# Kernel tuning notes

Measured on AMD Instinct MI355X. Metric: run time of the kernel, lower is better.

The kernel has to match this reference:

```python
import jax, jax.numpy as jnp
import numpy as np

N_QUBITS = 10
N_QLAYERS = 2
EMBED = 1024
B, S = 16, 1024
DIM = 2 ** N_QUBITS


def _apply_rx(state, theta, w, n):
    # state: [N, 2^n] complex; RX(theta) on wire w (wire 0 = most significant bit)
    nb = state.shape[0]
    left, right = 2 ** w, 2 ** (n - 1 - w)
    psi = state.reshape(nb, left, 2, right)
    t = jnp.asarray(theta, jnp.float32) * 0.5
    c, s = jnp.cos(t), jnp.sin(t)
    if c.ndim == 1:  # per-sample angles
        c, s = c[:, None, None], s[:, None, None]
    a0, a1 = psi[:, :, 0, :], psi[:, :, 1, :]
    n0 = c * a0 - 1j * s * a1
    n1 = -1j * s * a0 + c * a1
    return jnp.stack([n0, n1], axis=2).reshape(nb, -1)


def _apply_cnot(state, c, t, n):
    # CNOT with control wire c, target wire t
    psi = state.reshape((-1,) + (2,) * n)
    ctrl_ax, tgt_ax = c + 1, t + 1
    psi0, psi1 = jnp.split(psi, 2, axis=ctrl_ax)
    psi1 = jnp.flip(psi1, axis=tgt_ax)
    return jnp.concatenate([psi0, psi1], axis=ctrl_ax).reshape(state.shape)


def setup_inputs() -> dict:
    key = jax.random.key(0)
    ks = jax.random.split(key, 6)
    s1 = 1.0 / np.sqrt(EMBED)
    s2 = 1.0 / np.sqrt(N_QUBITS)
    return {
        "x": jax.random.normal(ks[0], (B, S, EMBED), jnp.float32),
        "W1": jax.random.uniform(ks[1], (N_QUBITS, EMBED), jnp.float32, -s1, s1),
        "b1": jax.random.uniform(ks[2], (N_QUBITS,), jnp.float32, -s1, s1),
        "qweights": jax.random.uniform(ks[3], (N_QLAYERS, N_QUBITS), jnp.float32, 0.0, 2.0 * np.pi),
        "W2": jax.random.uniform(ks[4], (EMBED, N_QUBITS), jnp.float32, -s2, s2),
        "b2": jax.random.uniform(ks[5], (EMBED,), jnp.float32, -s2, s2),
    }


def reference(x, W1, b1, qweights, W2, b2):
    n = N_QUBITS
    # linear_1
    ang = (jnp.einsum('bse,qe->bsq', x, W1) + b1).reshape(-1, n)  # [N, n]
    N = ang.shape[0]
    # |0...0> batched state vector
    state = jnp.zeros((N, DIM), jnp.complex64).at[:, 0].set(1.0)
    # AngleEmbedding: RX(ang[:, w]) on each wire
    for w in range(n):
        state = _apply_rx(state, ang[:, w], w, n)
    # BasicEntanglerLayers: RX rotations + CNOT ring per layer
    for l in range(N_QLAYERS):
        for w in range(n):
            state = _apply_rx(state, qweights[l, w], w, n)
        if n == 2:
            state = _apply_cnot(state, 0, 1, n)
        elif n > 2:
            for i in range(n):
                state = _apply_cnot(state, i, (i + 1) % n, n)
    # <Z_w> = sum_idx probs[idx] * (1 - 2*bit_w(idx))
    probs = jnp.real(state * jnp.conj(state))  # [N, 2^n]
    idx = jnp.arange(DIM)
    bits = (idx[:, None] >> (n - 1 - jnp.arange(n))[None, :]) & 1
    signs = (1 - 2 * bits).astype(jnp.float32)  # [2^n, n]
    ev = (probs @ signs).reshape(x.shape[0], x.shape[1], n)  # [B, S, n]
    # linear_2
    return jnp.einsum('bsq,eq->bse', ev, W2) + b2
```

## Files before the change

### kernel.cpp

```cpp
#include <hip/hip_runtime.h>

#define NQ 10
#define EMBED 1024
#define ROWS_PER_BLOCK 32
#define BLOCK 512


constexpr int kPop(int x) { int c = 0; for (int i = 0; i < 10; ++i) c += (x >> i) & 1; return c; }

constexpr int sigma_map(int a) {
    int b = 0;
    for (int i = 0; i < 9; ++i) b |= (((a >> i) & 1) ^ ((a >> (i + 1)) & 1)) << i;
    b |= (((a >> 9) & 1) ^ ((a >> 0) & 1) ^ ((a >> 1) & 1)) << 9;
    return b;
}

#define MAXT 40
struct Terms {
    int nt[NQ];
    int vm[NQ];
    int um[NQ];
    unsigned short tm[NQ][MAXT];
    unsigned short sm[NQ][MAXT];
    float sg[NQ][MAXT];
};

constexpr Terms gen_terms() {
    Terms t{};
    int inv_e[NQ] = {};
    for (int a = 0; a < 1024; ++a) {
        const int s = sigma_map(a);
        for (int q = 0; q < NQ; ++q) if (s == (1 << q)) inv_e[q] = a;
    }
    for (int q = 0; q < NQ; ++q) {
        const int u = inv_e[q];
        int v = 0;
        for (int w = 0; w < NQ; ++w) if ((u >> w) & 1) v ^= inv_e[w];
        t.um[q] = u; t.vm[q] = v;
        int n = 0;
        int S = 0;
        while (true) {
            int T = (((S >> 0) ^ (S >> 9)) & 1)
                  | ((((S >> 0) ^ (S >> 1) ^ (S >> 9)) & 1) << 1);
            for (int j = 2; j < 10; ++j) T |= ((((S >> (j - 1)) ^ (S >> j)) & 1) << j);
            if ((T & ~v) == 0) {
                const int p = kPop(T) + kPop(S);
                if (!(p & 1)) {
                    t.tm[q][n] = (unsigned short)T;
                    t.sm[q][n] = (unsigned short)S;
                    t.sg[q][n] = (p & 2) ? -1.f : 1.f;
                    ++n;
                }
            }
            if (S == u) break;
            S = (S - u) & u;
        }
        t.nt[q] = n;
    }
    return t;
}

constexpr Terms TT = gen_terms();

template <int CTRL, int RM>
__device__ __forceinline__ float dppadd(float v) {
    const int s = __builtin_amdgcn_update_dpp(0, __float_as_int(v), CTRL, RM, 0xF, true);
    return v + __int_as_float(s);
}
__device__ __forceinline__ float red32(float v) {
    v = dppadd<0xB1,  0xF>(v);
    v = dppadd<0x4E,  0xF>(v);
    v = dppadd<0x141, 0xF>(v);
    v = dppadd<0x140, 0xF>(v);
    v = dppadd<0x142, 0xA>(v);
    return v;
}

extern "C" __global__ __launch_bounds__(BLOCK, 4)
void ffq_kernel(const float* __restrict__ x, const float* __restrict__ W1,
                const float* __restrict__ b1, const float* __restrict__ qw,
                const float* __restrict__ W2, const float* __restrict__ b2,
                float* __restrict__ out)
{
    __shared__ float sW1[NQ * EMBED];
    __shared__ float sCA[ROWS_PER_BLOCK][11];
    __shared__ float sSA[ROWS_PER_BLOCK][11];
    __shared__ float sEVv[ROWS_PER_BLOCK][11];

    const int tid  = threadIdx.x;
    const int lane = tid & 63;
    const int wv   = tid >> 6;
    const int o    = lane & 31;
    const int g    = lane >> 5;
    const int block0 = blockIdx.x * ROWS_PER_BLOCK;

    {
        const float4* src = (const float4*)W1;
        float4* dst = (float4*)sW1;
        #pragma unroll
        for (int i = 0; i < 5; ++i) dst[tid + BLOCK * i] = src[tid + BLOCK * i];
    }

    float b1q[NQ];
    #pragma unroll
    for (int w = 0; w < NQ; ++w) b1q[w] = b1[w] + qw[w];

    __syncthreads();

    {
        const int rloc0 = wv * 4 + g * 2;
        const float4* xr0 = (const float4*)(x + (size_t)(block0 + rloc0) * EMBED);
        const float4* xr1 = (const float4*)(x + (size_t)(block0 + rloc0 + 1) * EMBED);

        float4 xv0[8], xv1[8];
        #pragma unroll
        for (int k = 0; k < 8; ++k) xv0[k] = xr0[k * 32 + o];
        #pragma unroll
        for (int k = 0; k < 8; ++k) xv1[k] = xr1[k * 32 + o];

        float acc0[NQ], acc1[NQ];
        #pragma unroll
        for (int q = 0; q < NQ; ++q) { acc0[q] = 0.f; acc1[q] = 0.f; }

        const float4* w1v = (const float4*)sW1;
        #pragma unroll
        for (int k = 0; k < 8; ++k) {
            float4 wA[5];
            #pragma unroll
            for (int q = 0; q < 5; ++q) wA[q] = w1v[q * 256 + k * 32 + o];
            #pragma unroll
            for (int q = 0; q < 5; ++q) {
                acc0[q] = fmaf(xv0[k].x, wA[q].x, acc0[q]);
                acc0[q] = fmaf(xv0[k].y, wA[q].y, acc0[q]);
                acc0[q] = fmaf(xv0[k].z, wA[q].z, acc0[q]);
                acc0[q] = fmaf(xv0[k].w, wA[q].w, acc0[q]);
                acc1[q] = fmaf(xv1[k].x, wA[q].x, acc1[q]);
                acc1[q] = fmaf(xv1[k].y, wA[q].y, acc1[q]);
                acc1[q] = fmaf(xv1[k].z, wA[q].z, acc1[q]);
                acc1[q] = fmaf(xv1[k].w, wA[q].w, acc1[q]);
            }
            float4 wB[5];
            #pragma unroll
            for (int q = 0; q < 5; ++q) wB[q] = w1v[(5 + q) * 256 + k * 32 + o];
            #pragma unroll
            for (int q = 0; q < 5; ++q) {
                acc0[5+q] = fmaf(xv0[k].x, wB[q].x, acc0[5+q]);
                acc0[5+q] = fmaf(xv0[k].y, wB[q].y, acc0[5+q]);
                acc0[5+q] = fmaf(xv0[k].z, wB[q].z, acc0[5+q]);
                acc0[5+q] = fmaf(xv0[k].w, wB[q].w, acc0[5+q]);
                acc1[5+q] = fmaf(xv1[k].x, wB[q].x, acc1[5+q]);
                acc1[5+q] = fmaf(xv1[k].y, wB[q].y, acc1[5+q]);
                acc1[5+q] = fmaf(xv1[k].z, wB[q].z, acc1[5+q]);
                acc1[5+q] = fmaf(xv1[k].w, wB[q].w, acc1[5+q]);
            }
        }

        #pragma unroll
        for (int q = 0; q < NQ; ++q) {
            acc0[q] = red32(acc0[q]);
            acc1[q] = red32(acc1[q]);
        }

        if (o == 16) {
            #pragma unroll
            for (int w = 0; w < NQ; ++w) {
                const float A = acc0[w] + b1q[w];
                sCA[rloc0][w] = __cosf(A);
                sSA[rloc0][w] = __sinf(A);
            }
        } else if (o == 17) {
            #pragma unroll
            for (int w = 0; w < NQ; ++w) {
                const float A = acc1[w] + b1q[w];
                sCA[rloc0 + 1][w] = __cosf(A);
                sSA[rloc0 + 1][w] = __sinf(A);
            }
        }
    }

    const int e4 = tid & 255;
    float w2f[40];
    {
        const float4* w2v = (const float4*)(W2 + e4 * 40);
        #pragma unroll
        for (int i = 0; i < 10; ++i) {
            float4 v = w2v[i];
            w2f[4*i+0] = v.x; w2f[4*i+1] = v.y; w2f[4*i+2] = v.z; w2f[4*i+3] = v.w;
        }
    }
    const float4 b2v = ((const float4*)b2)[e4];

    __syncthreads();

    if (lane < ROWS_PER_BLOCK) {
        const int row = lane;
        float ca[NQ], sa[NQ], cb[NQ], sb[NQ];
        #pragma unroll
        for (int w = 0; w < NQ; ++w) {
            ca[w] = sCA[row][w];
            sa[w] = sSA[row][w];
            const float B = qw[NQ + w];
            cb[w] = __cosf(B); sb[w] = __sinf(B);
        }
        #define EVQ(QC) do {                                                      \
            float ev = 0.f;                                                       \
            _Pragma("unroll")                                                     \
            for (int k = 0; k < TT.nt[QC]; ++k) {                                 \
                float P = TT.sg[QC][k];                                           \
                _Pragma("unroll")                                                 \
                for (int w = 0; w < NQ; ++w) {                                    \
                    if ((TT.vm[QC] >> w) & 1) P *= ((TT.tm[QC][k] >> w) & 1) ? sa[w] : ca[w]; \
                    if ((TT.um[QC] >> w) & 1) P *= ((TT.sm[QC][k] >> w) & 1) ? sb[w] : cb[w]; \
                }                                                                 \
                ev += P;                                                          \
            }                                                                     \
            sEVv[row][QC] = ev;                                                   \
        } while (0)
        switch (wv) {
            case 0: EVQ(0); break;
            case 1: EVQ(9); break;
            case 2: EVQ(7); break;
            case 3: EVQ(8); break;
            case 4: EVQ(5); EVQ(6); break;
            case 5: EVQ(3); EVQ(4); break;
            case 6: EVQ(1); EVQ(2); break;
            default: break;
        }
        #undef EVQ
    }

    __syncthreads();

    const int r0 = (tid >> 8) * 16;
    #pragma unroll
    for (int r = 0; r < 16; ++r) {
        const int rr = r0 + r;
        float evr[NQ];
        #pragma unroll
        for (int q = 0; q < NQ; ++q) evr[q] = sEVv[rr][q];
        float o0 = b2v.x, o1 = b2v.y, o2 = b2v.z, o3 = b2v.w;
        #pragma unroll
        for (int q = 0; q < NQ; ++q) {
            o0 = fmaf(evr[q], w2f[ 0 + q], o0);
            o1 = fmaf(evr[q], w2f[10 + q], o1);
            o2 = fmaf(evr[q], w2f[20 + q], o2);
            o3 = fmaf(evr[q], w2f[30 + q], o3);
        }
        float4 ov = {o0, o1, o2, o3};
        ((float4*)(out + (size_t)(block0 + rr) * EMBED))[e4] = ov;
    }
}

extern "C" void kernel_launch(void* const* d_in, const int* in_sizes, int n_in,
                              void* d_out, int out_size, void* d_ws, size_t ws_size,
                              hipStream_t stream) {
    (void)in_sizes; (void)n_in; (void)d_ws; (void)ws_size; (void)out_size;
    const float* x  = (const float*)d_in[0];
    const float* W1 = (const float*)d_in[1];
    const float* b1 = (const float*)d_in[2];
    const float* qw = (const float*)d_in[3];
    const float* W2 = (const float*)d_in[4];
    const float* b2 = (const float*)d_in[5];
    float* out = (float*)d_out;

    const int total_rows = 16 * 1024;
    dim3 grid(total_rows / ROWS_PER_BLOCK);
    ffq_kernel<<<grid, BLOCK, 0, stream>>>(x, W1, b1, qw, W2, b2, out);
}
```

Baseline: 28.27 us.

## Use full 64-lane waves over four rows in linear_1 with double-buffered x loads

The first linear layer now has each wavefront handle four rows across all 64 lanes, instead of two half-waves handling two rows each. Each W1 value read from shared memory is therefore reused for four rows, halving LDS traffic per FMA. The x loads are split into two alternating buffers that are refilled between k-steps so global loads overlap compute. The reduction gains a sixth DPP step (row_bcast31) to sum across the full wave. The cost is more accumulator registers (40 instead of 20), which may pressure occupancy under the 4-blocks launch bound.

Measured after the change: 33.73 us. +19.3%, slower.

```diff
diff --git a/kernel.cpp b/kernel.cpp
--- a/kernel.cpp
+++ b/kernel.cpp
@@ -67,14 +67,21 @@
     const int s = __builtin_amdgcn_update_dpp(0, __float_as_int(v), CTRL, RM, 0xF, true);
     return v + __int_as_float(s);
 }
-__device__ __forceinline__ float red32(float v) {
+__device__ __forceinline__ float red64(float v) {
     v = dppadd<0xB1,  0xF>(v);
     v = dppadd<0x4E,  0xF>(v);
     v = dppadd<0x141, 0xF>(v);
     v = dppadd<0x140, 0xF>(v);
     v = dppadd<0x142, 0xA>(v);
+    v = dppadd<0x143, 0x8>(v);
     return v;
 }
+
+#define FMA1(ACC, XV, WW)                 \
+    ACC = fmaf((XV).x, (WW).x, ACC);      \
+    ACC = fmaf((XV).y, (WW).y, ACC);      \
+    ACC = fmaf((XV).z, (WW).z, ACC);      \
+    ACC = fmaf((XV).w, (WW).w, ACC);
 
 extern "C" __global__ __launch_bounds__(BLOCK, 4)
 void ffq_kernel(const float* __restrict__ x, const float* __restrict__ W1,
@@ -90,8 +97,6 @@
     const int tid  = threadIdx.x;
     const int lane = tid & 63;
     const int wv   = tid >> 6;
-    const int o    = lane & 31;
-    const int g    = lane >> 5;
     const int block0 = blockIdx.x * ROWS_PER_BLOCK;
 
     {
@@ -108,72 +113,69 @@
     __syncthreads();
 
     {
-        const int rloc0 = wv * 4 + g * 2;
-        const float4* xr0 = (const float4*)(x + (size_t)(block0 + rloc0) * EMBED);
-        const float4* xr1 = (const float4*)(x + (size_t)(block0 + rloc0 + 1) * EMBED);
-
-        float4 xv0[8], xv1[8];
-        #pragma unroll
-        for (int k = 0; k < 8; ++k) xv0[k] = xr0[k * 32 + o];
-        #pragma unroll
-        for (int k = 0; k < 8; ++k) xv1[k] = xr1[k * 32 + o];
-
-        float acc0[NQ], acc1[NQ];
-        #pragma unroll
-        for (int q = 0; q < NQ; ++q) { acc0[q] = 0.f; acc1[q] = 0.f; }
+        const int rbase = wv * 4;
+        const float4* xr0 = (const float4*)(x + (size_t)(block0 + rbase + 0) * EMBED);
+        const float4* xr1 = (const float4*)(x + (size_t)(block0 + rbase + 1) * EMBED);
+        const float4* xr2 = (const float4*)(x + (size_t)(block0 + rbase + 2) * EMBED);
+        const float4* xr3 = (const float4*)(x + (size_t)(block0 + rbase + 3) * EMBED);
+
+        float4 xa0 = xr0[lane],      xa1 = xr1[lane],      xa2 = xr2[lane],      xa3 = xr3[lane];
+        float4 xb0 = xr0[64 + lane], xb1 = xr1[64 + lane], xb2 = xr2[64 + lane], xb3 = xr3[64 + lane];
+
+        float acc0[NQ], acc1[NQ], acc2[NQ], acc3[NQ];
+        #pragma unroll
+        for (int q = 0; q < NQ; ++q) { acc0[q] = 0.f; acc1[q] = 0.f; acc2[q] = 0.f; acc3[q] = 0.f; }
 
         const float4* w1v = (const float4*)sW1;
-        #pragma unroll
-        for (int k = 0; k < 8; ++k) {
-            float4 wA[5];
-            #pragma unroll
-            for (int q = 0; q < 5; ++q) wA[q] = w1v[q * 256 + k * 32 + o];
-            #pragma unroll
-            for (int q = 0; q < 5; ++q) {
-                acc0[q] = fmaf(xv0[k].x, wA[q].x, acc0[q]);
-                acc0[q] = fmaf(xv0[k].y, wA[q].y, acc0[q]);
-                acc0[q] = fmaf(xv0[k].z, wA[q].z, acc0[q]);
-                acc0[q] = fmaf(xv0[k].w, wA[q].w, acc0[q]);
-                acc1[q] = fmaf(xv1[k].x, wA[q].x, acc1[q]);
-                acc1[q] = fmaf(xv1[k].y, wA[q].y, acc1[q]);
-                acc1[q] = fmaf(xv1[k].z, wA[q].z, acc1[q]);
-                acc1[q] = fmaf(xv1[k].w, wA[q].w, acc1[q]);
-            }
-            float4 wB[5];
-            #pragma unroll
-            for (int q = 0; q < 5; ++q) wB[q] = w1v[(5 + q) * 256 + k * 32 + o];
-            #pragma unroll
-            for (int q = 0; q < 5; ++q) {
-                acc0[5+q] = fmaf(xv0[k].x, wB[q].x, acc0[5+q]);
-                acc0[5+q] = fmaf(xv0[k].y, wB[q].y, acc0[5+q]);
-                acc0[5+q] = fmaf(xv0[k].z, wB[q].z, acc0[5+q]);
-                acc0[5+q] = fmaf(xv0[k].w, wB[q].w, acc0[5+q]);
-                acc1[5+q] = fmaf(xv1[k].x, wB[q].x, acc1[5+q]);
-                acc1[5+q] = fmaf(xv1[k].y, wB[q].y, acc1[5+q]);
-                acc1[5+q] = fmaf(xv1[k].z, wB[q].z, acc1[5+q]);
-                acc1[5+q] = fmaf(xv1[k].w, wB[q].w, acc1[5+q]);
-            }
-        }
+
+        #define KSTEP(X0, X1, X2, X3, K) do {                                   \
+            float4 wA[5];                                                        \
+            _Pragma("unroll")                                                    \
+            for (int q = 0; q < 5; ++q) wA[q] = w1v[q * 256 + (K) * 64 + lane];  \
+            _Pragma("unroll")                                                    \
+            for (int q = 0; q < 5; ++q) {                                        \
+                FMA1(acc0[q], X0, wA[q]); FMA1(acc1[q], X1, wA[q]);              \
+                FMA1(acc2[q], X2, wA[q]); FMA1(acc3[q], X3, wA[q]);              \
+            }                                                                    \
+            float4 wB[5];                                                        \
+            _Pragma("unroll")                                                    \
+            for (int q = 0; q < 5; ++q) wB[q] = w1v[(5 + q) * 256 + (K) * 64 + lane]; \
+            _Pragma("unroll")                                                    \
+            for (int q = 0; q < 5; ++q) {                                        \
+                FMA1(acc0[5+q], X0, wB[q]); FMA1(acc1[5+q], X1, wB[q]);          \
+                FMA1(acc2[5+q], X2, wB[q]); FMA1(acc3[5+q], X3, wB[q]);          \
+            }                                                                    \
+        } while (0)
+
+        KSTEP(xa0, xa1, xa2, xa3, 0);
+        xa0 = xr0[2 * 64 + lane]; xa1 = xr1[2 * 64 + lane];
+        xa2 = xr2[2 * 64 + lane]; xa3 = xr3[2 * 64 + lane];
+        KSTEP(xb0, xb1, xb2, xb3, 1);
+        xb0 = xr0[3 * 64 + lane]; xb1 = xr1[3 * 64 + lane];
+        xb2 = xr2[3 * 64 + lane]; xb3 = xr3[3 * 64 + lane];
+        KSTEP(xa0, xa1, xa2, xa3, 2);
+        KSTEP(xb0, xb1, xb2, xb3, 3);
+        #undef KSTEP
 
         #pragma unroll
         for (int q = 0; q < NQ; ++q) {
-            acc0[q] = red32(acc0[q]);
-            acc1[q] = red32(acc1[q]);
-        }
-
-        if (o == 16) {
+            acc0[q] = red64(acc0[q]);
+            acc1[q] = red64(acc1[q]);
+            acc2[q] = red64(acc2[q]);
+            acc3[q] = red64(acc3[q]);
+        }
+
+        if (lane >= 48 && lane < 52) {
+            const int rr = lane & 3;
             #pragma unroll
             for (int w = 0; w < NQ; ++w) {
-                const float A = acc0[w] + b1q[w];
-                sCA[rloc0][w] = __cosf(A);
-                sSA[rloc0][w] = __sinf(A);
-            }
-        } else if (o == 17) {
-            #pragma unroll
-            for (int w = 0; w < NQ; ++w) {
-                const float A = acc1[w] + b1q[w];
-                sCA[rloc0 + 1][w] = __cosf(A);
-                sSA[rloc0 + 1][w] = __sinf(A);
+                float v = acc0[w];
+                v = (rr == 1) ? acc1[w] : v;
+                v = (rr == 2) ? acc2[w] : v;
+                v = (rr == 3) ? acc3[w] : v;
+                const float A = v + b1q[w];
+                sCA[rbase + rr][w] = __cosf(A);
+                sSA[rbase + rr][w] = __sinf(A);
             }
         }
     }
```
